# Kernel tuning notes

Measured on AMD Instinct MI355X. Metric: run time of the kernel, lower is better.

## Reference

```python
import jax, jax.numpy as jnp
import numpy as np

B, T, D, H = 4, 2048, 1024, 16
Dh = D // H


def setup_inputs() -> dict:
    key = jax.random.key(0)
    ks = jax.random.split(key, 10)
    s = 0.02  # init scale for weights
    return {
        "x": jax.random.normal(ks[0], (B, T, D), jnp.float32),
        "gates": jax.random.uniform(ks[1], (B, H), jnp.float32),
        "Wq": jax.random.normal(ks[2], (D, D), jnp.float32) * s,
        "bq": jnp.zeros((D,), jnp.float32),
        "Wk": jax.random.normal(ks[3], (D, D), jnp.float32) * s,
        "bk": jnp.zeros((D,), jnp.float32),
        "Wv": jax.random.normal(ks[4], (D, D), jnp.float32) * s,
        "bv": jnp.zeros((D,), jnp.float32),
        "Wo": jax.random.normal(ks[5], (D, D), jnp.float32) * s,
        "bo": jnp.zeros((D,), jnp.float32),
    }


def reference(x, gates, Wq, bq, Wk, bk, Wv, bv, Wo, bo):
    # x: [B,T,D], gates: [B,H]. torch Linear is y = x @ W.T + b.
    b, t, d = x.shape
    h = gates.shape[1]
    dh = d // h
    q = (x @ Wq.T + bq).reshape(b, t, h, dh)
    k = (x @ Wk.T + bk).reshape(b, t, h, dh)
    v = (x @ Wv.T + bv).reshape(b, t, h, dh)
    scores = jnp.einsum('bthd,bshd->bhts', q, k) / jnp.sqrt(jnp.float32(dh))
    A = jax.nn.softmax(scores, axis=-1)
    A = A * gates[:, :, None, None]  # post-softmax per-head gate
    z = jnp.einsum('bhts,bshd->bthd', A, v).reshape(b, t, d)
    out = z @ Wo.T + bo
    return out, A
```

## Files before the change

### kernel.cpp

```cpp
#include <hip/hip_runtime.h>

#define BB 4
#define TT 2048
#define DD 1024
#define HH 16
#define DHH 64

using half8  = __attribute__((ext_vector_type(8))) _Float16;
using half4v = __attribute__((ext_vector_type(4))) _Float16;
using f32x4  = __attribute__((ext_vector_type(4))) float;

#define EXP2C 0.18033688011112042f

__device__ __forceinline__ float fexp2(float x) {
#if __has_builtin(__builtin_amdgcn_exp2f)
  return __builtin_amdgcn_exp2f(x);
#else
  return exp2f(x);
#endif
}

__device__ __forceinline__ void gload_lds16(const _Float16* g, _Float16* l) {
  __builtin_amdgcn_global_load_lds((const __attribute__((address_space(1))) void*)g,
                                   (__attribute__((address_space(3))) void*)l, 16, 0, 0);
}

__global__ void cvt_all(const float* __restrict__ x,
                        const float* __restrict__ wq, const float* __restrict__ wk,
                        const float* __restrict__ wv, const float* __restrict__ wo,
                        _Float16* __restrict__ xh,
                        _Float16* __restrict__ wqh, _Float16* __restrict__ wkh,
                        _Float16* __restrict__ wvh, _Float16* __restrict__ woh) {
  const float* s; _Float16* d; int n8, b0, nb;
  int b = blockIdx.x;
  if (b < 512) { s = x; d = xh; n8 = BB * TT * DD / 8; b0 = b; nb = 512; }
  else {
    int wsel = (b - 512) >> 6;
    b0 = (b - 512) & 63; nb = 64; n8 = DD * DD / 8;
    s = wsel == 0 ? wq : wsel == 1 ? wk : wsel == 2 ? wv : wo;
    d = wsel == 0 ? wqh : wsel == 1 ? wkh : wsel == 2 ? wvh : woh;
  }
  for (int i = b0 * 256 + threadIdx.x; i < n8; i += nb * 256) {
    const float4* p = (const float4*)(s + (size_t)i * 8);
    float4 a = p[0], bb = p[1];
    half8 h;
    h[0] = (_Float16)a.x; h[1] = (_Float16)a.y; h[2] = (_Float16)a.z; h[3] = (_Float16)a.w;
    h[4] = (_Float16)bb.x; h[5] = (_Float16)bb.y; h[6] = (_Float16)bb.z; h[7] = (_Float16)bb.w;
    *(half8*)(d + (size_t)i * 8) = h;
  }
}

#define GEMM_STAGE(K0, BSEL)                                                        \
  _Pragma("unroll") for (int it = 0; it < 4; ++it) {                                \
    int chunk = tid + it * 256;                                                     \
    int r = chunk >> 3, pb = chunk & 7, lb = pb ^ (r & 7);                          \
    gload_lds16(A + (size_t)(row0 + r) * K + (K0) * 64 + lb * 8, As[BSEL] + chunk * 8);  \
    gload_lds16(Bw + (size_t)(col0 + r) * K + (K0) * 64 + lb * 8, Bs[BSEL] + chunk * 8); \
  }

__global__ __launch_bounds__(256, 2) void gemm_qkv(const _Float16* __restrict__ A,
                                                   const _Float16* __restrict__ Wqh,
                                                   const _Float16* __restrict__ Wkh,
                                                   const _Float16* __restrict__ Wvh,
                                                   const float* __restrict__ bq,
                                                   const float* __restrict__ bk,
                                                   const float* __restrict__ bv,
                                                   _Float16* __restrict__ qh,
                                                   _Float16* __restrict__ kh,
                                                   _Float16* __restrict__ vTh) {
  constexpr int K = 1024;
  __shared__ _Float16 As[2][128 * 64];
  __shared__ _Float16 Bs[2][128 * 64];
  const int tid = threadIdx.x;
  const int l = tid & 63, w = tid >> 6;
  const int wm = w >> 1, wn = w & 1;
  const int lg = l >> 4, lr16 = l & 15;
  const int wsel = (int)blockIdx.y >> 3;
  const _Float16* Bw = wsel == 0 ? Wqh : wsel == 1 ? Wkh : Wvh;
  const float* bias = wsel == 0 ? bq : wsel == 1 ? bk : bv;
  const int row0 = blockIdx.x * 128, col0 = ((int)blockIdx.y & 7) * 128;

  f32x4 acc[4][4];
#pragma unroll
  for (int i = 0; i < 4; ++i)
#pragma unroll
    for (int j = 0; j < 4; ++j) acc[i][j] = (f32x4)0.0f;

  GEMM_STAGE(0, 0);
  int cur = 0;
  for (int k0 = 0; k0 < 16; ++k0) {
    __syncthreads();
    if (k0 < 15) GEMM_STAGE(k0 + 1, cur ^ 1);
#pragma unroll
    for (int kb = 0; kb < 2; ++kb) {
      half8 a[4], b[4];
#pragma unroll
      for (int f = 0; f < 4; ++f) {
        int ar = wm * 64 + f * 16 + lr16;
        a[f] = *(const half8*)(As[cur] + ar * 64 + ((kb * 4 + lg) ^ (ar & 7)) * 8);
        int br = wn * 64 + f * 16 + lr16;
        b[f] = *(const half8*)(Bs[cur] + br * 64 + ((kb * 4 + lg) ^ (br & 7)) * 8);
      }
#pragma unroll
      for (int i = 0; i < 4; ++i)
#pragma unroll
        for (int j = 0; j < 4; ++j)
          acc[i][j] = __builtin_amdgcn_mfma_f32_16x16x32_f16(a[i], b[j], acc[i][j], 0, 0, 0);
    }
    cur ^= 1;
  }

#pragma unroll
  for (int fi = 0; fi < 4; ++fi) {
#pragma unroll
    for (int fj = 0; fj < 4; ++fj) {
      int gi0 = row0 + wm * 64 + fi * 16 + lg * 4;
      int gj = col0 + wn * 64 + fj * 16 + lr16;
      float bj = bias[gj];
      int b = gi0 >> 11, t0 = gi0 & 2047;
      int h = gj >> 6, dh = gj & 63;
      if (wsel < 2) {
        _Float16* O = wsel ? kh : qh;
#pragma unroll
        for (int r = 0; r < 4; ++r)
          O[(((size_t)(b * HH + h) * TT + (t0 + r)) << 6) + dh] = (_Float16)(acc[fi][fj][r] + bj);
      } else {
        half4v tmp;
#pragma unroll
        for (int r = 0; r < 4; ++r) tmp[r] = (_Float16)(acc[fi][fj][r] + bj);
        *(half4v*)(vTh + (((size_t)(b * HH + h) * DHH + dh) * TT + t0)) = tmp;
      }
    }
  }
}

__global__ __launch_bounds__(256, 2) void gemm_out(const _Float16* __restrict__ A,
                                                   const _Float16* __restrict__ Bw,
                                                   const float* __restrict__ bias,
                                                   float* __restrict__ Cout) {
  constexpr int K = 1024;
  __shared__ _Float16 As[2][128 * 64];
  __shared__ _Float16 Bs[2][128 * 64];
  const int tid = threadIdx.x;
  const int l = tid & 63, w = tid >> 6;
  const int wm = w >> 1, wn = w & 1;
  const int lg = l >> 4, lr16 = l & 15;
  const int row0 = blockIdx.x * 128, col0 = blockIdx.y * 128;

  f32x4 acc[4][4];
#pragma unroll
  for (int i = 0; i < 4; ++i)
#pragma unroll
    for (int j = 0; j < 4; ++j) acc[i][j] = (f32x4)0.0f;

  GEMM_STAGE(0, 0);
  int cur = 0;
  for (int k0 = 0; k0 < 16; ++k0) {
    __syncthreads();
    if (k0 < 15) GEMM_STAGE(k0 + 1, cur ^ 1);
#pragma unroll
    for (int kb = 0; kb < 2; ++kb) {
      half8 a[4], b[4];
#pragma unroll
      for (int f = 0; f < 4; ++f) {
        int ar = wm * 64 + f * 16 + lr16;
        a[f] = *(const half8*)(As[cur] + ar * 64 + ((kb * 4 + lg) ^ (ar & 7)) * 8);
        int br = wn * 64 + f * 16 + lr16;
        b[f] = *(const half8*)(Bs[cur] + br * 64 + ((kb * 4 + lg) ^ (br & 7)) * 8);
      }
#pragma unroll
      for (int i = 0; i < 4; ++i)
#pragma unroll
        for (int j = 0; j < 4; ++j)
          acc[i][j] = __builtin_amdgcn_mfma_f32_16x16x32_f16(a[i], b[j], acc[i][j], 0, 0, 0);
    }
    cur ^= 1;
  }

#pragma unroll
  for (int fi = 0; fi < 4; ++fi) {
#pragma unroll
    for (int fj = 0; fj < 4; ++fj) {
      int gi0 = row0 + wm * 64 + fi * 16 + lg * 4;
      int gj = col0 + wn * 64 + fj * 16 + lr16;
      float bj = bias[gj];
#pragma unroll
      for (int r = 0; r < 4; ++r)
        __builtin_nontemporal_store(acc[fi][fj][r] + bj, &Cout[(size_t)(gi0 + r) * DD + gj]);
    }
  }
}

__global__ __launch_bounds__(512, 2) void attn_kernel(const _Float16* __restrict__ qh,
                                                      const _Float16* __restrict__ kh,
                                                      const _Float16* __restrict__ vTh,
                                                      const float* __restrict__ gates,
                                                      float* __restrict__ Aout,
                                                      _Float16* __restrict__ zh) {
  __shared__ _Float16 Qs[128 * 64];
  __shared__ _Float16 Ks[2][64 * 64];
  __shared__ _Float16 Vs[2][64 * 64];
  __shared__ _Float16 Ps[128 * 64];
  const int tid = threadIdx.x;
  const int l = tid & 63, w = tid >> 6;
  const int lg = l >> 4, lr16 = l & 15;
  const int wr0 = w * 16;
  const int blk = ((int)blockIdx.x & 7) * 128 + ((int)blockIdx.x >> 3);
  const int rt = blk & 15, bh = blk >> 4;
  const _Float16* Qp = qh + (size_t)bh * TT * DHH + (size_t)rt * 128 * DHH;
  const _Float16* Kp = kh + (size_t)bh * TT * DHH;
  const _Float16* Vp = vTh + (size_t)bh * DHH * TT;
  float* Ap = Aout + (size_t)bh * TT * TT + (size_t)rt * 128 * TT;
  const float gate = gates[bh];

#pragma unroll
  for (int it = 0; it < 2; ++it) {
    int chunk = tid + it * 512;
    int r = chunk >> 3, pb = chunk & 7, lb = pb ^ (r & 7);
    gload_lds16(Qp + (size_t)r * DHH + lb * 8, Qs + chunk * 8);
  }

#define STAGE_K(CT, BSEL) {                                                   \
    int chunk = tid; int r = chunk >> 3, pb = chunk & 7, lb = pb ^ (r & 7);   \
    gload_lds16(Kp + (size_t)((CT) * 64 + r) * DHH + lb * 8, Ks[BSEL] + chunk * 8); }
#define STAGE_V(CT, BSEL) {                                                   \
    int chunk = tid; int r = chunk >> 3, pb = chunk & 7, lb = pb ^ (r & 7);   \
    gload_lds16(Vp + (size_t)r * TT + (CT) * 64 + lb * 8, Vs[BSEL] + chunk * 8); }

  STAGE_K(0, 0);
  float rs = 0.f;
  int cur = 0;
  for (int ct = 0; ct < 32; ++ct) {
    __syncthreads();
    if (ct < 31) STAGE_K(ct + 1, cur ^ 1);
    f32x4 s[4];
#pragma unroll
    for (int j = 0; j < 4; ++j) s[j] = (f32x4)0.0f;
    __builtin_amdgcn_s_setprio(1);
#pragma unroll
    for (int kb = 0; kb < 2; ++kb) {
      int qr = wr0 + lr16;
      half8 aQ = *(const half8*)(Qs + qr * 64 + (((kb * 4 + lg) ^ (qr & 7)) * 8));
      half8 bK[4];
#pragma unroll
      for (int fc = 0; fc < 4; ++fc) {
        int kr = fc * 16 + lr16;
        bK[fc] = *(const half8*)(Ks[cur] + kr * 64 + (((kb * 4 + lg) ^ (kr & 7)) * 8));
      }
#pragma unroll
      for (int fc = 0; fc < 4; ++fc)
        s[fc] = __builtin_amdgcn_mfma_f32_16x16x32_f16(bK[fc], aQ, s[fc], 0, 0, 0);
    }
    __builtin_amdgcn_s_setprio(0);
#pragma unroll
    for (int fc = 0; fc < 4; ++fc)
#pragma unroll
      for (int r = 0; r < 4; ++r) rs += fexp2(s[fc][r] * EXP2C);
    cur ^= 1;
  }

  {
    rs += __shfl_xor(rs, 16, 64);
    rs += __shfl_xor(rs, 32, 64);
  }
  const float inv = gate / rs;

  f32x4 z[4];
#pragma unroll
  for (int j = 0; j < 4; ++j) z[j] = (f32x4)0.0f;
  STAGE_K(0, 0);
  STAGE_V(0, 0);
  asm volatile("s_waitcnt vmcnt(0)\n\ts_barrier" ::: "memory");
  cur = 0;
  for (int ct = 0; ct < 32; ++ct) {
    if (ct < 31) {
      STAGE_K(ct + 1, cur ^ 1);
      STAGE_V(ct + 1, cur ^ 1);
    }
    __builtin_amdgcn_sched_barrier(0);
    f32x4 s[4];
#pragma unroll
    for (int j = 0; j < 4; ++j) s[j] = (f32x4)0.0f;
    __builtin_amdgcn_s_setprio(1);
#pragma unroll
    for (int kb = 0; kb < 2; ++kb) {
      int qr = wr0 + lr16;
      half8 aQ = *(const half8*)(Qs + qr * 64 + (((kb * 4 + lg) ^ (qr & 7)) * 8));
      half8 bK[4];
#pragma unroll
      for (int fc = 0; fc < 4; ++fc) {
        int kr = fc * 16 + lr16;
        bK[fc] = *(const half8*)(Ks[cur] + kr * 64 + (((kb * 4 + lg) ^ (kr & 7)) * 8));
      }
#pragma unroll
      for (int fc = 0; fc < 4; ++fc)
        s[fc] = __builtin_amdgcn_mfma_f32_16x16x32_f16(bK[fc], aQ, s[fc], 0, 0, 0);
    }
    __builtin_amdgcn_s_setprio(0);
    const int q = wr0 + lr16;
#pragma unroll
    for (int fc = 0; fc < 4; ++fc) {
      f32x4 o;
      half4v ph;
#pragma unroll
      for (int r = 0; r < 4; ++r) {
        float av = fexp2(s[fc][r] * EXP2C) * inv;
        o[r] = av;
        ph[r] = (_Float16)av;
      }
      __builtin_nontemporal_store(o, (f32x4*)(Ap + (size_t)q * TT + ct * 64 + fc * 16 + lg * 4));
      int g8 = fc * 2 + (lg >> 1);
      *(half4v*)(Ps + q * 64 + ((g8 ^ (q & 7)) * 8) + (lg & 1) * 4) = ph;
    }
    __builtin_amdgcn_s_setprio(1);
#pragma unroll
    for (int kb = 0; kb < 2; ++kb) {
      int pr = wr0 + lr16;
      half8 aP = *(const half8*)(Ps + pr * 64 + (((kb * 4 + lg) ^ (pr & 7)) * 8));
      half8 bV[4];
#pragma unroll
      for (int fc = 0; fc < 4; ++fc) {
        int vr = fc * 16 + lr16;
        bV[fc] = *(const half8*)(Vs[cur] + vr * 64 + (((kb * 4 + lg) ^ (vr & 7)) * 8));
      }
#pragma unroll
      for (int fc = 0; fc < 4; ++fc)
        z[fc] = __builtin_amdgcn_mfma_f32_16x16x32_f16(aP, bV[fc], z[fc], 0, 0, 0);
    }
    __builtin_amdgcn_s_setprio(0);
    if (ct < 31) {
      asm volatile("s_waitcnt vmcnt(4) lgkmcnt(0)\n\ts_barrier" ::: "memory");
    }
    cur ^= 1;
  }

  const int b = bh >> 4, h = bh & 15;
  _Float16* zp = zh + ((size_t)b * TT + (size_t)rt * 128) * DD + h * 64;
  const int rbase = wr0 + lg * 4;
#pragma unroll
  for (int fc = 0; fc < 4; ++fc) {
    int d = fc * 16 + lr16;
#pragma unroll
    for (int r = 0; r < 4; ++r) zp[(size_t)(rbase + r) * DD + d] = (_Float16)z[fc][r];
  }
}

extern "C" void kernel_launch(void* const* d_in, const int* in_sizes, int n_in,
                              void* d_out, int out_size, void* d_ws, size_t ws_size,
                              hipStream_t stream) {
  const float* x     = (const float*)d_in[0];
  const float* gates = (const float*)d_in[1];
  const float* Wq    = (const float*)d_in[2];
  const float* bq    = (const float*)d_in[3];
  const float* Wk    = (const float*)d_in[4];
  const float* bk    = (const float*)d_in[5];
  const float* Wv    = (const float*)d_in[6];
  const float* bv    = (const float*)d_in[7];
  const float* Wo    = (const float*)d_in[8];
  const float* bo    = (const float*)d_in[9];

  float* out  = (float*)d_out;
  float* Aout = out + (size_t)BB * TT * DD;

  char* ws = (char*)d_ws;
  _Float16* xh  = (_Float16*)(ws);
  _Float16* Wqh = (_Float16*)(ws + (16ull << 20));
  _Float16* Wkh = (_Float16*)(ws + (18ull << 20));
  _Float16* Wvh = (_Float16*)(ws + (20ull << 20));
  _Float16* Woh = (_Float16*)(ws + (22ull << 20));
  _Float16* qh  = (_Float16*)(ws + (24ull << 20));
  _Float16* kh  = (_Float16*)(ws + (40ull << 20));
  _Float16* vTh = (_Float16*)(ws + (56ull << 20));
  _Float16* zh  = xh;

  cvt_all<<<768, 256, 0, stream>>>(x, Wq, Wk, Wv, Wo, xh, Wqh, Wkh, Wvh, Woh);

  gemm_qkv<<<dim3(BB * TT / 128, 24), 256, 0, stream>>>(xh, Wqh, Wkh, Wvh, bq, bk, bv,
                                                        qh, kh, vTh);

  attn_kernel<<<BB * HH * (TT / 128), 512, 0, stream>>>(qh, kh, vTh, gates, Aout, zh);

  gemm_out<<<dim3(BB * TT / 128, DD / 128), 256, 0, stream>>>(zh, Woh, bo, out);
}
```

Measured before the change: 459.3 us.

## Triple-buffer K/V tiles in attention and keep Q fragments in registers

```diff
diff --git a/kernel.cpp b/kernel.cpp
--- a/kernel.cpp
+++ b/kernel.cpp
@@ -197,9 +197,8 @@
                                                       const float* __restrict__ gates,
                                                       float* __restrict__ Aout,
                                                       _Float16* __restrict__ zh) {
-  __shared__ _Float16 Qs[128 * 64];
-  __shared__ _Float16 Ks[2][64 * 64];
-  __shared__ _Float16 Vs[2][64 * 64];
+  __shared__ _Float16 Ks[3][64 * 64];
+  __shared__ _Float16 Vs[3][64 * 64];
   __shared__ _Float16 Ps[128 * 64];
   const int tid = threadIdx.x;
   const int l = tid & 63, w = tid >> 6;
@@ -213,39 +212,49 @@
   float* Ap = Aout + (size_t)bh * TT * TT + (size_t)rt * 128 * TT;
   const float gate = gates[bh];
 
-#pragma unroll
-  for (int it = 0; it < 2; ++it) {
-    int chunk = tid + it * 512;
-    int r = chunk >> 3, pb = chunk & 7, lb = pb ^ (r & 7);
-    gload_lds16(Qp + (size_t)r * DHH + lb * 8, Qs + chunk * 8);
-  }
+  {
+    _Float16* Qscratch = Ks[0];
+#pragma unroll
+    for (int it = 0; it < 2; ++it) {
+      int chunk = tid + it * 512;
+      int r = chunk >> 3, pb = chunk & 7, lb = pb ^ (r & 7);
+      gload_lds16(Qp + (size_t)r * DHH + lb * 8, Qscratch + chunk * 8);
+    }
+  }
+  __syncthreads();
+  const int qr = wr0 + lr16;
+  const half8 aQ0 = *(const half8*)(Ks[0] + qr * 64 + ((lg ^ (qr & 7)) * 8));
+  const half8 aQ1 = *(const half8*)(Ks[0] + qr * 64 + (((4 + lg) ^ (qr & 7)) * 8));
+  __syncthreads();
 
 #define STAGE_K(CT, BSEL) {                                                   \
-    int chunk = tid; int r = chunk >> 3, pb = chunk & 7, lb = pb ^ (r & 7);   \
-    gload_lds16(Kp + (size_t)((CT) * 64 + r) * DHH + lb * 8, Ks[BSEL] + chunk * 8); }
+    int r = tid >> 3, pb = tid & 7, lb = pb ^ (r & 7);                        \
+    gload_lds16(Kp + (size_t)((CT) * 64 + r) * DHH + lb * 8, Ks[BSEL] + tid * 8); }
 #define STAGE_V(CT, BSEL) {                                                   \
-    int chunk = tid; int r = chunk >> 3, pb = chunk & 7, lb = pb ^ (r & 7);   \
-    gload_lds16(Vp + (size_t)r * TT + (CT) * 64 + lb * 8, Vs[BSEL] + chunk * 8); }
+    int r = tid >> 3, pb = tid & 7, lb = pb ^ (r & 7);                        \
+    gload_lds16(Vp + (size_t)r * TT + (CT) * 64 + lb * 8, Vs[BSEL] + tid * 8); }
 
   STAGE_K(0, 0);
+  STAGE_K(1, 1);
+  asm volatile("s_waitcnt vmcnt(1)\n\ts_barrier" ::: "memory");
   float rs = 0.f;
-  int cur = 0;
+  int bc = 0;
   for (int ct = 0; ct < 32; ++ct) {
-    __syncthreads();
-    if (ct < 31) STAGE_K(ct + 1, cur ^ 1);
+    int bp = bc + 2; if (bp >= 3) bp -= 3;
+    if (ct < 30) STAGE_K(ct + 2, bp);
+    __builtin_amdgcn_sched_barrier(0);
     f32x4 s[4];
 #pragma unroll
     for (int j = 0; j < 4; ++j) s[j] = (f32x4)0.0f;
     __builtin_amdgcn_s_setprio(1);
 #pragma unroll
     for (int kb = 0; kb < 2; ++kb) {
-      int qr = wr0 + lr16;
-      half8 aQ = *(const half8*)(Qs + qr * 64 + (((kb * 4 + lg) ^ (qr & 7)) * 8));
+      half8 aQ = kb ? aQ1 : aQ0;
       half8 bK[4];
 #pragma unroll
       for (int fc = 0; fc < 4; ++fc) {
         int kr = fc * 16 + lr16;
-        bK[fc] = *(const half8*)(Ks[cur] + kr * 64 + (((kb * 4 + lg) ^ (kr & 7)) * 8));
+        bK[fc] = *(const half8*)(Ks[bc] + kr * 64 + (((kb * 4 + lg) ^ (kr & 7)) * 8));
       }
 #pragma unroll
       for (int fc = 0; fc < 4; ++fc)
@@ -256,26 +265,33 @@
     for (int fc = 0; fc < 4; ++fc)
 #pragma unroll
       for (int r = 0; r < 4; ++r) rs += fexp2(s[fc][r] * EXP2C);
-    cur ^= 1;
-  }
-
-  {
-    rs += __shfl_xor(rs, 16, 64);
-    rs += __shfl_xor(rs, 32, 64);
-  }
+    if (ct < 30) {
+      asm volatile("s_waitcnt vmcnt(1) lgkmcnt(0)\n\ts_barrier" ::: "memory");
+    } else if (ct == 30) {
+      asm volatile("s_waitcnt vmcnt(0) lgkmcnt(0)\n\ts_barrier" ::: "memory");
+    }
+    bc = bc + 1; if (bc >= 3) bc -= 3;
+  }
+
+  rs += __shfl_xor(rs, 16, 64);
+  rs += __shfl_xor(rs, 32, 64);
   const float inv = gate / rs;
+  __syncthreads();
 
   f32x4 z[4];
 #pragma unroll
   for (int j = 0; j < 4; ++j) z[j] = (f32x4)0.0f;
   STAGE_K(0, 0);
   STAGE_V(0, 0);
-  asm volatile("s_waitcnt vmcnt(0)\n\ts_barrier" ::: "memory");
-  cur = 0;
+  STAGE_K(1, 1);
+  STAGE_V(1, 1);
+  asm volatile("s_waitcnt vmcnt(2)\n\ts_barrier" ::: "memory");
+  bc = 0;
   for (int ct = 0; ct < 32; ++ct) {
-    if (ct < 31) {
-      STAGE_K(ct + 1, cur ^ 1);
-      STAGE_V(ct + 1, cur ^ 1);
+    int bp = bc + 2; if (bp >= 3) bp -= 3;
+    if (ct < 30) {
+      STAGE_K(ct + 2, bp);
+      STAGE_V(ct + 2, bp);
     }
     __builtin_amdgcn_sched_barrier(0);
     f32x4 s[4];
@@ -284,13 +300,12 @@
     __builtin_amdgcn_s_setprio(1);
 #pragma unroll
     for (int kb = 0; kb < 2; ++kb) {
-      int qr = wr0 + lr16;
-      half8 aQ = *(const half8*)(Qs + qr * 64 + (((kb * 4 + lg) ^ (qr & 7)) * 8));
+      half8 aQ = kb ? aQ1 : aQ0;
       half8 bK[4];
 #pragma unroll
       for (int fc = 0; fc < 4; ++fc) {
         int kr = fc * 16 + lr16;
-        bK[fc] = *(const half8*)(Ks[cur] + kr * 64 + (((kb * 4 + lg) ^ (kr & 7)) * 8));
+        bK[fc] = *(const half8*)(Ks[bc] + kr * 64 + (((kb * 4 + lg) ^ (kr & 7)) * 8));
       }
 #pragma unroll
       for (int fc = 0; fc < 4; ++fc)
@@ -321,17 +336,21 @@
 #pragma unroll
       for (int fc = 0; fc < 4; ++fc) {
         int vr = fc * 16 + lr16;
-        bV[fc] = *(const half8*)(Vs[cur] + vr * 64 + (((kb * 4 + lg) ^ (vr & 7)) * 8));
+        bV[fc] = *(const half8*)(Vs[bc] + vr * 64 + (((kb * 4 + lg) ^ (vr & 7)) * 8));
       }
 #pragma unroll
       for (int fc = 0; fc < 4; ++fc)
         z[fc] = __builtin_amdgcn_mfma_f32_16x16x32_f16(aP, bV[fc], z[fc], 0, 0, 0);
     }
     __builtin_amdgcn_s_setprio(0);
-    if (ct < 31) {
-      asm volatile("s_waitcnt vmcnt(4) lgkmcnt(0)\n\ts_barrier" ::: "memory");
-    }
-    cur ^= 1;
+    if (ct == 0) {
+      asm volatile("s_waitcnt vmcnt(6) lgkmcnt(0)\n\ts_barrier" ::: "memory");
+    } else if (ct < 30) {
+      asm volatile("s_waitcnt vmcnt(10) lgkmcnt(0)\n\ts_barrier" ::: "memory");
+    } else if (ct == 30) {
+      asm volatile("s_waitcnt vmcnt(8) lgkmcnt(0)\n\ts_barrier" ::: "memory");
+    }
+    bc = bc + 1; if (bc >= 3) bc -= 3;
   }
 
   const int b = bh >> 4, h = bh & 15;
```

New measurement: 455.4 us. No clear change (-0.8%).

## Widen attention key tiles to 128, keep Q in registers, drop nontemporal stores

Applied to the files above, without the earlier changes.

```diff
diff --git a/kernel.cpp b/kernel.cpp
--- a/kernel.cpp
+++ b/kernel.cpp
@@ -186,21 +186,20 @@
       float bj = bias[gj];
 #pragma unroll
       for (int r = 0; r < 4; ++r)
-        __builtin_nontemporal_store(acc[fi][fj][r] + bj, &Cout[(size_t)(gi0 + r) * DD + gj]);
-    }
-  }
-}
-
-__global__ __launch_bounds__(512, 2) void attn_kernel(const _Float16* __restrict__ qh,
+        Cout[(size_t)(gi0 + r) * DD + gj] = acc[fi][fj][r] + bj;
+    }
+  }
+}
+
+__global__ __launch_bounds__(512, 1) void attn_kernel(const _Float16* __restrict__ qh,
                                                       const _Float16* __restrict__ kh,
                                                       const _Float16* __restrict__ vTh,
                                                       const float* __restrict__ gates,
                                                       float* __restrict__ Aout,
                                                       _Float16* __restrict__ zh) {
-  __shared__ _Float16 Qs[128 * 64];
-  __shared__ _Float16 Ks[2][64 * 64];
-  __shared__ _Float16 Vs[2][64 * 64];
-  __shared__ _Float16 Ps[128 * 64];
+  __shared__ _Float16 Ks[2][128 * 64];
+  __shared__ _Float16 Vs[2][64 * 128];
+  __shared__ _Float16 Ps[128 * 128];
   const int tid = threadIdx.x;
   const int l = tid & 63, w = tid >> 6;
   const int lg = l >> 4, lr16 = l & 15;
@@ -213,57 +212,71 @@
   float* Ap = Aout + (size_t)bh * TT * TT + (size_t)rt * 128 * TT;
   const float gate = gates[bh];
 
-#pragma unroll
-  for (int it = 0; it < 2; ++it) {
-    int chunk = tid + it * 512;
-    int r = chunk >> 3, pb = chunk & 7, lb = pb ^ (r & 7);
-    gload_lds16(Qp + (size_t)r * DHH + lb * 8, Qs + chunk * 8);
-  }
-
-#define STAGE_K(CT, BSEL) {                                                   \
-    int chunk = tid; int r = chunk >> 3, pb = chunk & 7, lb = pb ^ (r & 7);   \
-    gload_lds16(Kp + (size_t)((CT) * 64 + r) * DHH + lb * 8, Ks[BSEL] + chunk * 8); }
-#define STAGE_V(CT, BSEL) {                                                   \
-    int chunk = tid; int r = chunk >> 3, pb = chunk & 7, lb = pb ^ (r & 7);   \
-    gload_lds16(Vp + (size_t)r * TT + (CT) * 64 + lb * 8, Vs[BSEL] + chunk * 8); }
+  {
+    _Float16* Qscratch = Ks[0];
+#pragma unroll
+    for (int it = 0; it < 2; ++it) {
+      int chunk = tid + it * 512;
+      int r = chunk >> 3, pb = chunk & 7, lb = pb ^ (r & 7);
+      gload_lds16(Qp + (size_t)r * DHH + lb * 8, Qscratch + chunk * 8);
+    }
+  }
+  __syncthreads();
+  const int qr = wr0 + lr16;
+  const half8 aQ0 = *(const half8*)(Ks[0] + qr * 64 + ((lg ^ (qr & 7)) * 8));
+  const half8 aQ1 = *(const half8*)(Ks[0] + qr * 64 + (((4 + lg) ^ (qr & 7)) * 8));
+  __syncthreads();
+
+#define STAGE_K(CT, BSEL)                                                       \
+  _Pragma("unroll") for (int it = 0; it < 2; ++it) {                            \
+    int chunk = tid + it * 512;                                                 \
+    int r = chunk >> 3, pb = chunk & 7, lb = pb ^ (r & 7);                      \
+    gload_lds16(Kp + (size_t)((CT) * 128 + r) * DHH + lb * 8, Ks[BSEL] + chunk * 8); }
+#define STAGE_V(CT, BSEL)                                                       \
+  _Pragma("unroll") for (int it = 0; it < 2; ++it) {                            \
+    int chunk = tid + it * 512;                                                 \
+    int r = chunk >> 4, pc = chunk & 15, lb = pc ^ (r & 15);                    \
+    gload_lds16(Vp + (size_t)r * TT + (CT) * 128 + lb * 8, Vs[BSEL] + chunk * 8); }
 
   STAGE_K(0, 0);
+  asm volatile("s_waitcnt vmcnt(0)\n\ts_barrier" ::: "memory");
   float rs = 0.f;
   int cur = 0;
-  for (int ct = 0; ct < 32; ++ct) {
-    __syncthreads();
-    if (ct < 31) STAGE_K(ct + 1, cur ^ 1);
-    f32x4 s[4];
-#pragma unroll
-    for (int j = 0; j < 4; ++j) s[j] = (f32x4)0.0f;
+  for (int ct = 0; ct < 16; ++ct) {
+    if (ct < 15) STAGE_K(ct + 1, cur ^ 1);
+    __builtin_amdgcn_sched_barrier(0);
+    f32x4 s[8];
+#pragma unroll
+    for (int j = 0; j < 8; ++j) s[j] = (f32x4)0.0f;
     __builtin_amdgcn_s_setprio(1);
 #pragma unroll
     for (int kb = 0; kb < 2; ++kb) {
-      int qr = wr0 + lr16;
-      half8 aQ = *(const half8*)(Qs + qr * 64 + (((kb * 4 + lg) ^ (qr & 7)) * 8));
-      half8 bK[4];
-#pragma unroll
-      for (int fc = 0; fc < 4; ++fc) {
+      half8 aQ = kb ? aQ1 : aQ0;
+      half8 bK[8];
+#pragma unroll
+      for (int fc = 0; fc < 8; ++fc) {
         int kr = fc * 16 + lr16;
         bK[fc] = *(const half8*)(Ks[cur] + kr * 64 + (((kb * 4 + lg) ^ (kr & 7)) * 8));
       }
 #pragma unroll
-      for (int fc = 0; fc < 4; ++fc)
+      for (int fc = 0; fc < 8; ++fc)
         s[fc] = __builtin_amdgcn_mfma_f32_16x16x32_f16(bK[fc], aQ, s[fc], 0, 0, 0);
     }
     __builtin_amdgcn_s_setprio(0);
 #pragma unroll
-    for (int fc = 0; fc < 4; ++fc)
+    for (int fc = 0; fc < 8; ++fc)
 #pragma unroll
       for (int r = 0; r < 4; ++r) rs += fexp2(s[fc][r] * EXP2C);
+    if (ct < 15) {
+      asm volatile("s_waitcnt vmcnt(0) lgkmcnt(0)\n\ts_barrier" ::: "memory");
+    }
     cur ^= 1;
   }
 
-  {
-    rs += __shfl_xor(rs, 16, 64);
-    rs += __shfl_xor(rs, 32, 64);
-  }
+  rs += __shfl_xor(rs, 16, 64);
+  rs += __shfl_xor(rs, 32, 64);
   const float inv = gate / rs;
+  __syncthreads();
 
   f32x4 z[4];
 #pragma unroll
@@ -272,34 +285,33 @@
   STAGE_V(0, 0);
   asm volatile("s_waitcnt vmcnt(0)\n\ts_barrier" ::: "memory");
   cur = 0;
-  for (int ct = 0; ct < 32; ++ct) {
-    if (ct < 31) {
+  for (int ct = 0; ct < 16; ++ct) {
+    if (ct < 15) {
       STAGE_K(ct + 1, cur ^ 1);
       STAGE_V(ct + 1, cur ^ 1);
     }
     __builtin_amdgcn_sched_barrier(0);
-    f32x4 s[4];
-#pragma unroll
-    for (int j = 0; j < 4; ++j) s[j] = (f32x4)0.0f;
+    f32x4 s[8];
+#pragma unroll
+    for (int j = 0; j < 8; ++j) s[j] = (f32x4)0.0f;
     __builtin_amdgcn_s_setprio(1);
 #pragma unroll
     for (int kb = 0; kb < 2; ++kb) {
-      int qr = wr0 + lr16;
-      half8 aQ = *(const half8*)(Qs + qr * 64 + (((kb * 4 + lg) ^ (qr & 7)) * 8));
-      half8 bK[4];
-#pragma unroll
-      for (int fc = 0; fc < 4; ++fc) {
+      half8 aQ = kb ? aQ1 : aQ0;
+      half8 bK[8];
+#pragma unroll
+      for (int fc = 0; fc < 8; ++fc) {
         int kr = fc * 16 + lr16;
         bK[fc] = *(const half8*)(Ks[cur] + kr * 64 + (((kb * 4 + lg) ^ (kr & 7)) * 8));
       }
 #pragma unroll
-      for (int fc = 0; fc < 4; ++fc)
+      for (int fc = 0; fc < 8; ++fc)
         s[fc] = __builtin_amdgcn_mfma_f32_16x16x32_f16(bK[fc], aQ, s[fc], 0, 0, 0);
     }
     __builtin_amdgcn_s_setprio(0);
     const int q = wr0 + lr16;
 #pragma unroll
-    for (int fc = 0; fc < 4; ++fc) {
+    for (int fc = 0; fc < 8; ++fc) {
       f32x4 o;
       half4v ph;
 #pragma unroll
@@ -308,28 +320,28 @@
         o[r] = av;
         ph[r] = (_Float16)av;
       }
-      __builtin_nontemporal_store(o, (f32x4*)(Ap + (size_t)q * TT + ct * 64 + fc * 16 + lg * 4));
+      *(f32x4*)(Ap + (size_t)q * TT + ct * 128 + fc * 16 + lg * 4) = o;
       int g8 = fc * 2 + (lg >> 1);
-      *(half4v*)(Ps + q * 64 + ((g8 ^ (q & 7)) * 8) + (lg & 1) * 4) = ph;
+      *(half4v*)(Ps + q * 128 + ((g8 ^ (q & 15)) * 8) + (lg & 1) * 4) = ph;
     }
     __builtin_amdgcn_s_setprio(1);
 #pragma unroll
-    for (int kb = 0; kb < 2; ++kb) {
+    for (int kb2 = 0; kb2 < 4; ++kb2) {
       int pr = wr0 + lr16;
-      half8 aP = *(const half8*)(Ps + pr * 64 + (((kb * 4 + lg) ^ (pr & 7)) * 8));
+      half8 aP = *(const half8*)(Ps + pr * 128 + (((kb2 * 4 + lg) ^ (pr & 15)) * 8));
       half8 bV[4];
 #pragma unroll
       for (int fc = 0; fc < 4; ++fc) {
         int vr = fc * 16 + lr16;
-        bV[fc] = *(const half8*)(Vs[cur] + vr * 64 + (((kb * 4 + lg) ^ (vr & 7)) * 8));
+        bV[fc] = *(const half8*)(Vs[cur] + vr * 128 + (((kb2 * 4 + lg) ^ (vr & 15)) * 8));
       }
 #pragma unroll
       for (int fc = 0; fc < 4; ++fc)
         z[fc] = __builtin_amdgcn_mfma_f32_16x16x32_f16(aP, bV[fc], z[fc], 0, 0, 0);
     }
     __builtin_amdgcn_s_setprio(0);
-    if (ct < 31) {
-      asm volatile("s_waitcnt vmcnt(4) lgkmcnt(0)\n\ts_barrier" ::: "memory");
+    if (ct < 15) {
+      asm volatile("s_waitcnt vmcnt(8) lgkmcnt(0)\n\ts_barrier" ::: "memory");
     }
     cur ^= 1;
   }
```

Measured after the change: 468.6 us. 1.02x slower.

## Single-pass attention keeping unnormalized P row in LDS, deferred normalization

Applied to the files above, without the earlier changes.

```diff
diff --git a/kernel.cpp b/kernel.cpp
--- a/kernel.cpp
+++ b/kernel.cpp
@@ -186,162 +186,148 @@
       float bj = bias[gj];
 #pragma unroll
       for (int r = 0; r < 4; ++r)
-        __builtin_nontemporal_store(acc[fi][fj][r] + bj, &Cout[(size_t)(gi0 + r) * DD + gj]);
-    }
-  }
-}
-
-__global__ __launch_bounds__(512, 2) void attn_kernel(const _Float16* __restrict__ qh,
+        Cout[(size_t)(gi0 + r) * DD + gj] = acc[fi][fj][r] + bj;
+    }
+  }
+}
+
+__global__ __launch_bounds__(512, 1) void attn_kernel(const _Float16* __restrict__ qh,
                                                       const _Float16* __restrict__ kh,
                                                       const _Float16* __restrict__ vTh,
                                                       const float* __restrict__ gates,
                                                       float* __restrict__ Aout,
                                                       _Float16* __restrict__ zh) {
-  __shared__ _Float16 Qs[128 * 64];
-  __shared__ _Float16 Ks[2][64 * 64];
-  __shared__ _Float16 Vs[2][64 * 64];
-  __shared__ _Float16 Ps[128 * 64];
+  extern __shared__ char sm[];
+  _Float16* Sb = (_Float16*)sm;
+  _Float16* Ksm = (_Float16*)(sm + 131072);
+  _Float16* Vsm = (_Float16*)(sm + 147456);
+  float* rsscr  = (float*)(sm + 131072);
+  float* invscr = (float*)(sm + 131072 + 512);
+  float* zscr   = (float*)sm;
+
   const int tid = threadIdx.x;
   const int l = tid & 63, w = tid >> 6;
   const int lg = l >> 4, lr16 = l & 15;
-  const int wr0 = w * 16;
-  const int blk = ((int)blockIdx.x & 7) * 128 + ((int)blockIdx.x >> 3);
-  const int rt = blk & 15, bh = blk >> 4;
-  const _Float16* Qp = qh + (size_t)bh * TT * DHH + (size_t)rt * 128 * DHH;
+  const int wr = w >> 2, ws = w & 3;
+  const int blk = ((int)blockIdx.x & 7) * 512 + ((int)blockIdx.x >> 3);
+  const int rt = blk & 63, bh = blk >> 6;
+  const _Float16* Qp = qh + (size_t)bh * TT * DHH + (size_t)rt * 32 * DHH;
   const _Float16* Kp = kh + (size_t)bh * TT * DHH;
   const _Float16* Vp = vTh + (size_t)bh * DHH * TT;
-  float* Ap = Aout + (size_t)bh * TT * TT + (size_t)rt * 128 * TT;
   const float gate = gates[bh];
 
-#pragma unroll
-  for (int it = 0; it < 2; ++it) {
-    int chunk = tid + it * 512;
-    int r = chunk >> 3, pb = chunk & 7, lb = pb ^ (r & 7);
-    gload_lds16(Qp + (size_t)r * DHH + lb * 8, Qs + chunk * 8);
-  }
-
-#define STAGE_K(CT, BSEL) {                                                   \
-    int chunk = tid; int r = chunk >> 3, pb = chunk & 7, lb = pb ^ (r & 7);   \
-    gload_lds16(Kp + (size_t)((CT) * 64 + r) * DHH + lb * 8, Ks[BSEL] + chunk * 8); }
-#define STAGE_V(CT, BSEL) {                                                   \
-    int chunk = tid; int r = chunk >> 3, pb = chunk & 7, lb = pb ^ (r & 7);   \
-    gload_lds16(Vp + (size_t)r * TT + (CT) * 64 + lb * 8, Vs[BSEL] + chunk * 8); }
-
-  STAGE_K(0, 0);
-  float rs = 0.f;
-  int cur = 0;
-  for (int ct = 0; ct < 32; ++ct) {
-    __syncthreads();
-    if (ct < 31) STAGE_K(ct + 1, cur ^ 1);
-    f32x4 s[4];
-#pragma unroll
-    for (int j = 0; j < 4; ++j) s[j] = (f32x4)0.0f;
-    __builtin_amdgcn_s_setprio(1);
-#pragma unroll
-    for (int kb = 0; kb < 2; ++kb) {
-      int qr = wr0 + lr16;
-      half8 aQ = *(const half8*)(Qs + qr * 64 + (((kb * 4 + lg) ^ (qr & 7)) * 8));
-      half8 bK[4];
-#pragma unroll
-      for (int fc = 0; fc < 4; ++fc) {
-        int kr = fc * 16 + lr16;
-        bK[fc] = *(const half8*)(Ks[cur] + kr * 64 + (((kb * 4 + lg) ^ (kr & 7)) * 8));
-      }
-#pragma unroll
-      for (int fc = 0; fc < 4; ++fc)
-        s[fc] = __builtin_amdgcn_mfma_f32_16x16x32_f16(bK[fc], aQ, s[fc], 0, 0, 0);
-    }
-    __builtin_amdgcn_s_setprio(0);
-#pragma unroll
-    for (int fc = 0; fc < 4; ++fc)
-#pragma unroll
-      for (int r = 0; r < 4; ++r) rs += fexp2(s[fc][r] * EXP2C);
-    cur ^= 1;
-  }
-
-  {
-    rs += __shfl_xor(rs, 16, 64);
-    rs += __shfl_xor(rs, 32, 64);
-  }
-  const float inv = gate / rs;
-
-  f32x4 z[4];
-#pragma unroll
-  for (int j = 0; j < 4; ++j) z[j] = (f32x4)0.0f;
+  if (tid < 256) {
+    int r = tid >> 3, pb = tid & 7, lb = pb ^ (r & 7);
+    gload_lds16(Qp + (size_t)r * DHH + lb * 8, Ksm + tid * 8);
+  }
+  asm volatile("s_waitcnt vmcnt(0)" ::: "memory");
+  __syncthreads();
+  const int q32 = wr * 16 + lr16;
+  const half8 aQ0 = *(const half8*)(Ksm + q32 * 64 + ((lg ^ (q32 & 7)) * 8));
+  const half8 aQ1 = *(const half8*)(Ksm + q32 * 64 + (((4 + lg) ^ (q32 & 7)) * 8));
+  __syncthreads();
+
+#define STAGE_K(CT, BSEL) {                                                       \
+    int r = tid >> 3, pb = tid & 7, lb = pb ^ (r & 7);                            \
+    gload_lds16(Kp + (size_t)((CT) * 64 + r) * DHH + lb * 8,                      \
+                Ksm + (BSEL) * 4096 + tid * 8); }
+#define STAGE_V(CT, BSEL) {                                                       \
+    int r = tid >> 3, pb = tid & 7, lb = pb ^ (r & 7);                            \
+    gload_lds16(Vp + (size_t)r * TT + (CT) * 64 + lb * 8,                         \
+                Vsm + (BSEL) * 4096 + tid * 8); }
+
   STAGE_K(0, 0);
   STAGE_V(0, 0);
   asm volatile("s_waitcnt vmcnt(0)\n\ts_barrier" ::: "memory");
-  cur = 0;
+  float rs = 0.f;
+  f32x4 z[4];
+#pragma unroll
+  for (int j = 0; j < 4; ++j) z[j] = (f32x4)0.0f;
+  const int kr = ws * 16 + lr16;
+  int cur = 0;
   for (int ct = 0; ct < 32; ++ct) {
     if (ct < 31) {
       STAGE_K(ct + 1, cur ^ 1);
       STAGE_V(ct + 1, cur ^ 1);
     }
     __builtin_amdgcn_sched_barrier(0);
-    f32x4 s[4];
-#pragma unroll
-    for (int j = 0; j < 4; ++j) s[j] = (f32x4)0.0f;
+    const _Float16* Kc = Ksm + cur * 4096;
+    const _Float16* Vc = Vsm + cur * 4096;
+    f32x4 s = (f32x4)0.0f;
+    half8 bK0 = *(const half8*)(Kc + kr * 64 + ((lg ^ (kr & 7)) * 8));
+    half8 bK1 = *(const half8*)(Kc + kr * 64 + (((4 + lg) ^ (kr & 7)) * 8));
     __builtin_amdgcn_s_setprio(1);
-#pragma unroll
-    for (int kb = 0; kb < 2; ++kb) {
-      int qr = wr0 + lr16;
-      half8 aQ = *(const half8*)(Qs + qr * 64 + (((kb * 4 + lg) ^ (qr & 7)) * 8));
-      half8 bK[4];
-#pragma unroll
-      for (int fc = 0; fc < 4; ++fc) {
-        int kr = fc * 16 + lr16;
-        bK[fc] = *(const half8*)(Ks[cur] + kr * 64 + (((kb * 4 + lg) ^ (kr & 7)) * 8));
-      }
-#pragma unroll
-      for (int fc = 0; fc < 4; ++fc)
-        s[fc] = __builtin_amdgcn_mfma_f32_16x16x32_f16(bK[fc], aQ, s[fc], 0, 0, 0);
-    }
+    s = __builtin_amdgcn_mfma_f32_16x16x32_f16(bK0, aQ0, s, 0, 0, 0);
+    s = __builtin_amdgcn_mfma_f32_16x16x32_f16(bK1, aQ1, s, 0, 0, 0);
     __builtin_amdgcn_s_setprio(0);
-    const int q = wr0 + lr16;
-#pragma unroll
-    for (int fc = 0; fc < 4; ++fc) {
-      f32x4 o;
-      half4v ph;
-#pragma unroll
-      for (int r = 0; r < 4; ++r) {
-        float av = fexp2(s[fc][r] * EXP2C) * inv;
-        o[r] = av;
-        ph[r] = (_Float16)av;
-      }
-      __builtin_nontemporal_store(o, (f32x4*)(Ap + (size_t)q * TT + ct * 64 + fc * 16 + lg * 4));
-      int g8 = fc * 2 + (lg >> 1);
-      *(half4v*)(Ps + q * 64 + ((g8 ^ (q & 7)) * 8) + (lg & 1) * 4) = ph;
+    half4v ph;
+#pragma unroll
+    for (int j = 0; j < 4; ++j) {
+      float p = fexp2(s[j] * EXP2C);
+      rs += p;
+      ph[j] = (_Float16)p;
+    }
+    {
+      int g8 = ct * 8 + ws * 2 + (lg >> 1);
+      *(half4v*)(Sb + q32 * 2048 + ((g8 ^ (q32 & 15)) * 8) + (lg & 1) * 4) = ph;
     }
     __builtin_amdgcn_s_setprio(1);
 #pragma unroll
-    for (int kb = 0; kb < 2; ++kb) {
-      int pr = wr0 + lr16;
-      half8 aP = *(const half8*)(Ps + pr * 64 + (((kb * 4 + lg) ^ (pr & 7)) * 8));
-      half8 bV[4];
-#pragma unroll
-      for (int fc = 0; fc < 4; ++fc) {
-        int vr = fc * 16 + lr16;
-        bV[fc] = *(const half8*)(Vs[cur] + vr * 64 + (((kb * 4 + lg) ^ (vr & 7)) * 8));
-      }
-#pragma unroll
-      for (int fc = 0; fc < 4; ++fc)
-        z[fc] = __builtin_amdgcn_mfma_f32_16x16x32_f16(aP, bV[fc], z[fc], 0, 0, 0);
+    for (int fc2 = 0; fc2 < 4; ++fc2) {
+      int vr = fc2 * 16 + lr16;
+      half4v bV = *(const half4v*)(Vc + vr * 64 + (((ws * 2 + (lg >> 1)) ^ (vr & 7)) * 8) +
+                                   (lg & 1) * 4);
+      z[fc2] = __builtin_amdgcn_mfma_f32_16x16x16f16(ph, bV, z[fc2], 0, 0, 0);
     }
     __builtin_amdgcn_s_setprio(0);
-    if (ct < 31) {
-      asm volatile("s_waitcnt vmcnt(4) lgkmcnt(0)\n\ts_barrier" ::: "memory");
-    }
+    asm volatile("s_waitcnt vmcnt(0) lgkmcnt(0)\n\ts_barrier" ::: "memory");
     cur ^= 1;
   }
 
-  const int b = bh >> 4, h = bh & 15;
-  _Float16* zp = zh + ((size_t)b * TT + (size_t)rt * 128) * DD + h * 64;
-  const int rbase = wr0 + lg * 4;
-#pragma unroll
-  for (int fc = 0; fc < 4; ++fc) {
-    int d = fc * 16 + lr16;
-#pragma unroll
-    for (int r = 0; r < 4; ++r) zp[(size_t)(rbase + r) * DD + d] = (_Float16)z[fc][r];
+  rs += __shfl_xor(rs, 16, 64);
+  rs += __shfl_xor(rs, 32, 64);
+  if (lg == 0) rsscr[(wr * 4 + ws) * 16 + lr16] = rs;
+  __syncthreads();
+  {
+    float rtot = rsscr[(wr * 4 + 0) * 16 + lr16] + rsscr[(wr * 4 + 1) * 16 + lr16] +
+                 rsscr[(wr * 4 + 2) * 16 + lr16] + rsscr[(wr * 4 + 3) * 16 + lr16];
+    if (ws == 0 && lg == 0) invscr[wr * 16 + lr16] = gate / rtot;
+  }
+  __syncthreads();
+
+  {
+    float* Ab = Aout + (size_t)bh * TT * TT + (size_t)rt * 32 * TT;
+    for (int it = 0; it < 16; ++it) {
+      int flat = it * 4096 + tid * 8;
+      int q = flat >> 11, col = flat & 2047, g8 = col >> 3;
+      half8 v = *(const half8*)(Sb + q * 2048 + ((g8 ^ (q & 15)) * 8));
+      float iv = invscr[q];
+      f32x4 o0, o1;
+#pragma unroll
+      for (int k = 0; k < 4; ++k) { o0[k] = (float)v[k] * iv; o1[k] = (float)v[k + 4] * iv; }
+      *(f32x4*)(Ab + flat) = o0;
+      *(f32x4*)(Ab + flat + 4) = o1;
+    }
+  }
+  __syncthreads();
+
+#pragma unroll
+  for (int fc2 = 0; fc2 < 4; ++fc2)
+#pragma unroll
+    for (int j = 0; j < 4; ++j)
+      zscr[((size_t)ws * 32 + wr * 16 + lg * 4 + j) * 64 + fc2 * 16 + lr16] = z[fc2][j];
+  __syncthreads();
+  {
+    int q = tid >> 4, dh0 = (tid & 15) * 4;
+    f32x4 acc = (f32x4)0.0f;
+#pragma unroll
+    for (int s4 = 0; s4 < 4; ++s4) acc += *(const f32x4*)(zscr + ((size_t)s4 * 32 + q) * 64 + dh0);
+    float iv = invscr[q];
+    half4v hz;
+#pragma unroll
+    for (int k = 0; k < 4; ++k) hz[k] = (_Float16)(acc[k] * iv);
+    const int b = bh >> 4, h = bh & 15;
+    *(half4v*)(zh + ((size_t)(b * TT + rt * 32 + q)) * DD + h * 64 + dh0) = hz;
   }
 }
 
@@ -373,12 +359,19 @@
   _Float16* vTh = (_Float16*)(ws + (56ull << 20));
   _Float16* zh  = xh;
 
+  static bool smem_set = false;
+  if (!smem_set) {
+    (void)hipFuncSetAttribute((const void*)attn_kernel,
+                              hipFuncAttributeMaxDynamicSharedMemorySize, 163840);
+    smem_set = true;
+  }
+
   cvt_all<<<768, 256, 0, stream>>>(x, Wq, Wk, Wv, Wo, xh, Wqh, Wkh, Wvh, Woh);
 
   gemm_qkv<<<dim3(BB * TT / 128, 24), 256, 0, stream>>>(xh, Wqh, Wkh, Wvh, bq, bk, bv,
                                                         qh, kh, vTh);
 
-  attn_kernel<<<BB * HH * (TT / 128), 512, 0, stream>>>(qh, kh, vTh, gates, Aout, zh);
+  attn_kernel<<<BB * HH * (TT / 32), 512, 163840, stream>>>(qh, kh, vTh, gates, Aout, zh);
 
   gemm_out<<<dim3(BB * TT / 128, DD / 128), 256, 0, stream>>>(zh, Woh, bo, out);
 }
```

Result: slower. 646.6 us (+40.8%).
